# Performance work log

Measured on AMD Instinct MI355X. Metric: run time of the kernel, lower is better.

Reference implementation:

```python
import jax, jax.numpy as jnp
import numpy as np

B, D, S, F, C, H, OUT = 4, 60, 512, 158, 64, 128, 1
LN_EPS = 1e-5


def setup_inputs() -> dict:
    key = jax.random.key(0)
    ks = jax.random.split(key, 12)
    g = lambda k, shape, s=0.05: jax.random.normal(k, shape, dtype=jnp.float32) * s
    return dict(
        x=jax.random.normal(ks[0], (B, D, S, F), dtype=jnp.float32),
        feature_mask=jax.random.randint(ks[1], (B, D, S), 0, 2).astype(bool),
        wq=g(ks[2], (F, C)), bq=jnp.zeros((C,), jnp.float32),
        wk=g(ks[3], (F, C)), bk=jnp.zeros((C,), jnp.float32),
        wv=g(ks[4], (F, C)), bv=jnp.zeros((C,), jnp.float32),
        ln_g=jnp.ones((F + C,), jnp.float32), ln_b=jnp.zeros((F + C,), jnp.float32),
        w_ih=g(ks[5], (3 * H, F + C)), w_hh=g(ks[6], (3 * H, H)),
        b_ih=jnp.zeros((3 * H,), jnp.float32), b_hh=jnp.zeros((3 * H,), jnp.float32),
        w1=g(ks[7], (H, H // 2)), b1=jnp.zeros((H // 2,), jnp.float32),
        w2=g(ks[8], (H // 2, OUT)), b2=jnp.zeros((OUT,), jnp.float32),
    )


def reference(x, feature_mask, wq, bq, wk, bk, wv, bv, ln_g, ln_b,
              w_ih, w_hh, b_ih, b_hh, w1, b1, w2, b2):
    b, d, s, f = x.shape
    c = wq.shape[1]
    h_dim = w_hh.shape[1]

    # --- market context attention, vectorized over (batch, days) ---
    Q = x @ wq + bq            # (B,D,S,C)
    K = x @ wk + bk
    V = x @ wv + bv
    scores = jnp.einsum('bdsc,bdtc->bdst', Q, K) / jnp.sqrt(jnp.float32(c))
    scores = jnp.where(feature_mask[:, :, None, :], scores, -1e9)  # mask keys
    attn = jax.nn.softmax(scores, axis=-1)
    ctx = jnp.einsum('bdst,bdtc->bdsc', attn, V)       # (B,D,S,C)
    ctx = jnp.where(feature_mask[..., None], ctx, 0.0)  # mask queries
    denom = jnp.maximum(feature_mask.sum(axis=2), 1).astype(x.dtype)  # (B,D)
    market = ctx.sum(axis=2) / denom[..., None]         # (B,D,C)

    # --- concat + layernorm ---
    aug = jnp.concatenate(
        [x, jnp.broadcast_to(market[:, :, None, :], (b, d, s, c))], axis=-1)
    mu = aug.mean(-1, keepdims=True)
    var = aug.var(-1, keepdims=True)
    aug = (aug - mu) / jnp.sqrt(var + LN_EPS) * ln_g + ln_b  # (B,D,S,F+C)

    # --- GRU over days, batch = B*S independent sequences ---
    seq = aug.transpose(1, 0, 2, 3).reshape(d, b * s, f + c)  # (D, N, F+C)
    x_proj = seq @ w_ih.T + b_ih                               # (D, N, 3H)

    def step(h, xp):
        hp = h @ w_hh.T + b_hh
        xr, xz, xn = jnp.split(xp, 3, axis=-1)
        hr, hz, hn = jnp.split(hp, 3, axis=-1)
        r = jax.nn.sigmoid(xr + hr)
        z = jax.nn.sigmoid(xz + hz)
        n = jnp.tanh(xn + r * hn)
        return (1.0 - z) * n + z * h, None

    h0 = jnp.zeros((b * s, h_dim), x.dtype)
    h_last, _ = jax.lax.scan(step, h0, x_proj)  # last-step output
    h_last = h_last.reshape(b, s, h_dim)

    # --- output head (dropout inactive in eval) ---
    hid = jax.nn.relu(h_last @ w1 + b1)
    return hid @ w2 + b2  # (B, S, OUT)
```

## Files before the change

kernel.cpp:

```cpp
#include <hip/hip_runtime.h>
#include <hip/hip_bf16.h>
#include <math.h>

#define BB 4
#define DD 60
#define SS 512
#define FF 158
#define CC 64
#define HH 128
#define FC 222
#define G3 384
#define NN 2048
#define BDN 240

#define L2E  1.44269504f
#define L2E2 2.88539008f
#define QSCALE 0.18033688f

typedef _Float16 f16x8 __attribute__((ext_vector_type(8)));
typedef float f32x4 __attribute__((ext_vector_type(4)));

__device__ __forceinline__ float exp2_hw(float x){ return __builtin_amdgcn_exp2f(x); }
__device__ __forceinline__ float rcp_hw(float x){ return __builtin_amdgcn_rcpf(x); }

__global__ void prep_kernel(const float* __restrict__ w_ih,
                            const float* __restrict__ wq, const float* __restrict__ wk,
                            const float* __restrict__ wv, const float* __restrict__ w_hh,
                            _Float16* __restrict__ wf16, _Float16* __restrict__ wqkv,
                            _Float16* __restrict__ whh16){
    int idx = blockIdx.x*256 + threadIdx.x;
    if (idx < 384*224){
        int n = idx / 224, k = idx % 224;
        float sc = (n < 256) ? L2E : L2E2;
        wf16[idx] = (k < FC) ? (_Float16)(w_ih[n*FC + k] * sc) : (_Float16)0.0f;
    } else if (idx < 384*224 + 192*160){
        int i2 = idx - 384*224;
        int n = i2 / 160, k = i2 % 160;
        float v = 0.0f;
        if (k < FF){
            if (n < 64)       v = wq[k*CC + n];
            else if (n < 128) v = wk[k*CC + (n-64)];
            else              v = wv[k*CC + (n-128)];
        }
        wqkv[i2] = (_Float16)v;
    } else {
        int i3 = idx - (384*224 + 192*160);
        if (i3 < 384*128){
            int n = i3 / 128;
            float sc = (n < 256) ? L2E : L2E2;
            whh16[i3] = (_Float16)(w_hh[i3] * sc);
        }
    }
}

__global__ __launch_bounds__(256) void qkv_kernel(const float* __restrict__ x,
                           const _Float16* __restrict__ wqkv,
                           const float* __restrict__ bq, const float* __restrict__ bk,
                           const float* __restrict__ bv,
                           _Float16* __restrict__ Qh, _Float16* __restrict__ Kh,
                           float* __restrict__ V){
    __shared__ _Float16 xa[5][64][40];
    int tid  = threadIdx.x;
    int lane = tid & 63, wv = tid >> 6;
    int col  = lane & 15, quad = lane >> 4;
    int row0 = blockIdx.x * 64;

    f16x8 bfr[3][5];
    #pragma unroll
    for (int nt = 0; nt < 3; ++nt){
        int n = wv*48 + nt*16 + col;
        #pragma unroll
        for (int kq = 0; kq < 5; ++kq)
            bfr[nt][kq] = *(const f16x8*)&wqkv[n*160 + kq*32 + quad*8];
    }

    for (int i = tid; i < 64*160; i += 256){
        int r = i / 160, k = i % 160;
        float v = (k < FF) ? x[(size_t)(row0 + r)*FF + k] : 0.0f;
        xa[k >> 5][r][k & 31] = (_Float16)v;
    }
    __syncthreads();

    float bias[3];
    #pragma unroll
    for (int nt = 0; nt < 3; ++nt){
        int n = wv*48 + nt*16 + col;
        bias[nt] = (n < 64) ? bq[n] : (n < 128 ? bk[n-64] : bv[n-128]);
    }

    #pragma unroll 1
    for (int mt = 0; mt < 4; ++mt){
        f16x8 a[5];
        #pragma unroll
        for (int kq = 0; kq < 5; ++kq)
            a[kq] = *(const f16x8*)&xa[kq][mt*16 + col][quad*8];
        #pragma unroll
        for (int nt = 0; nt < 3; ++nt){
            f32x4 c = {0.0f, 0.0f, 0.0f, 0.0f};
            #pragma unroll
            for (int kq = 0; kq < 5; ++kq)
                c = __builtin_amdgcn_mfma_f32_16x16x32_f16(a[kq], bfr[nt][kq], c, 0, 0, 0);
            int n = wv*48 + nt*16 + col;
            #pragma unroll
            for (int reg = 0; reg < 4; ++reg){
                int row = row0 + mt*16 + quad*4 + reg;
                float val = c[reg] + bias[nt];
                if (n < 64)       Qh[(size_t)row*CC + n]       = (_Float16)(val * QSCALE);
                else if (n < 128) Kh[(size_t)row*CC + (n-64)]  = (_Float16)val;
                else              V [(size_t)row*CC + (n-128)] = val;
            }
        }
    }
}

__global__ __launch_bounds__(512) void attn_kernel(const _Float16* __restrict__ Qh,
                                                   const _Float16* __restrict__ Kh,
                                                   const int* __restrict__ mask,
                                                   const float* __restrict__ V,
                                                   float* __restrict__ market){
    __shared__ _Float16 kf[2][512][32];
    __shared__ float w_sh[512];
    __shared__ float mk_lds[512];

    int tid  = threadIdx.x;
    int bd   = blockIdx.x;
    int lane = tid & 63, wv = tid >> 6;
    int col  = lane & 15, quad = lane >> 4;

    const _Float16* qb = Qh + (size_t)(bd*SS)*CC;
    const _Float16* kb = Kh + (size_t)(bd*SS)*CC;

    {
        int t = tid;
        w_sh[t] = 0.0f;
        mk_lds[t] = (mask[bd*SS + t] != 0) ? 1.0f : 0.0f;
    }
    for (int i = tid; i < 4096; i += 512){
        int t = i >> 3, ch = i & 7;
        *(f16x8*)&kf[ch >> 2][t][(ch & 3)*8] = *(const f16x8*)&kb[t*CC + ch*8];
    }

    f16x8 a0[4], a1[4];
    #pragma unroll
    for (int af = 0; af < 4; ++af){
        int row = wv*64 + af*16 + col;
        a0[af] = *(const f16x8*)&qb[row*CC + quad*8];
        a1[af] = *(const f16x8*)&qb[row*CC + 32 + quad*8];
    }
    __syncthreads();

    float lacc[4][4] = {{0,0,0,0},{0,0,0,0},{0,0,0,0},{0,0,0,0}};
    #pragma unroll 2
    for (int kt = 0; kt < 32; ++kt){
        f16x8 b0 = *(const f16x8*)&kf[0][kt*16 + col][quad*8];
        f16x8 b1 = *(const f16x8*)&kf[1][kt*16 + col][quad*8];
        float mkv = mk_lds[kt*16 + col];
        #pragma unroll
        for (int af = 0; af < 4; ++af){
            f32x4 c = {0.0f, 0.0f, 0.0f, 0.0f};
            c = __builtin_amdgcn_mfma_f32_16x16x32_f16(a0[af], b0, c, 0, 0, 0);
            c = __builtin_amdgcn_mfma_f32_16x16x32_f16(a1[af], b1, c, 0, 0, 0);
            #pragma unroll
            for (int reg = 0; reg < 4; ++reg)
                lacc[af][reg] += exp2_hw(c[reg]) * mkv;
        }
    }
    float crv[4][4];
    #pragma unroll
    for (int af = 0; af < 4; ++af){
        #pragma unroll
        for (int reg = 0; reg < 4; ++reg){
            float l = lacc[af][reg];
            l += __shfl_xor(l, 1, 64);
            l += __shfl_xor(l, 2, 64);
            l += __shfl_xor(l, 4, 64);
            l += __shfl_xor(l, 8, 64);
            int row = wv*64 + af*16 + quad*4 + reg;
            crv[af][reg] = mk_lds[row] * rcp_hw(l);
        }
    }

    #pragma unroll 2
    for (int kt = 0; kt < 32; ++kt){
        f16x8 b0 = *(const f16x8*)&kf[0][kt*16 + col][quad*8];
        f16x8 b1 = *(const f16x8*)&kf[1][kt*16 + col][quad*8];
        float s = 0.0f;
        #pragma unroll
        for (int af = 0; af < 4; ++af){
            f32x4 c = {0.0f, 0.0f, 0.0f, 0.0f};
            c = __builtin_amdgcn_mfma_f32_16x16x32_f16(a0[af], b0, c, 0, 0, 0);
            c = __builtin_amdgcn_mfma_f32_16x16x32_f16(a1[af], b1, c, 0, 0, 0);
            #pragma unroll
            for (int reg = 0; reg < 4; ++reg)
                s = fmaf(exp2_hw(c[reg]), crv[af][reg], s);
        }
        s += __shfl_xor(s, 16, 64);
        s += __shfl_xor(s, 32, 64);
        if (quad == 0)
            atomicAdd(&w_sh[kt*16 + col], s);
    }
    __syncthreads();

    float* msum = (float*)kf;
    {
        int c = tid & 63, grp = tid >> 6;
        const float* vb = V + (size_t)(bd*SS)*CC;
        float acc = 0.0f;
        int t0 = grp*64;
        #pragma unroll 4
        for (int t = t0; t < t0 + 64; ++t)
            acc = fmaf(w_sh[t]*mk_lds[t], vb[(size_t)t*CC + c], acc);
        msum[grp*64 + c] = acc;
    }
    __syncthreads();
    if (tid < 64){
        float s = 0.0f;
        #pragma unroll
        for (int g = 0; g < 8; ++g) s += msum[g*64 + tid];
        float cnt = 0.0f;
        #pragma unroll
        for (int j = 0; j < 8; ++j) cnt += mk_lds[tid + 64*j];
        #pragma unroll
        for (int o = 1; o < 64; o <<= 1) cnt += __shfl_xor(cnt, o, 64);
        market[bd*CC + tid] = s * rcp_hw(fmaxf(cnt, 1.0f));
    }
}

__global__ __launch_bounds__(512, 2) void xproj_kernel(const float* __restrict__ x,
                             const float* __restrict__ market,
                             const float* __restrict__ ln_g, const float* __restrict__ ln_b,
                             const _Float16* __restrict__ wf16, const float* __restrict__ b_ih,
                             _Float16* __restrict__ XP){
    __shared__ _Float16 aug[7][64][32];
    int tid  = threadIdx.x;
    int lane = tid & 63, wv = tid >> 6;
    int col  = lane & 15, quad = lane >> 4;
    int row0 = blockIdx.x * 64;

    f16x8 bfr[3][7];
    #pragma unroll
    for (int nt = 0; nt < 3; ++nt){
        int n = wv*48 + nt*16 + col;
        #pragma unroll
        for (int kq = 0; kq < 7; ++kq)
            bfr[nt][kq] = *(const f16x8*)&wf16[n*224 + kq*32 + quad*8];
    }

    {
        int wrow = wv*8 + (lane >> 3);
        int g    = lane & 7;
        int row  = row0 + wrow;
        int d = row / NN, n = row % NN;
        int b = n >> 9, s = n & 511;
        const float* xr = &x[((size_t)((b*DD + d)*SS) + s)*FF];
        const float* mr = &market[(b*DD + d)*CC];
        float v[28];
        float sum = 0.0f, sq = 0.0f;
        #pragma unroll
        for (int j = 0; j < 28; ++j){
            int f = g + 8*j;
            float vv = 0.0f;
            if (f < FF) vv = xr[f];
            else if (f < FC) vv = mr[f - FF];
            v[j] = vv;
            sum += vv; sq += vv*vv;
        }
        sum += __shfl_xor(sum,1,64); sq += __shfl_xor(sq,1,64);
        sum += __shfl_xor(sum,2,64); sq += __shfl_xor(sq,2,64);
        sum += __shfl_xor(sum,4,64); sq += __shfl_xor(sq,4,64);
        float mu   = sum * (1.0f/222.0f);
        float var  = sq * (1.0f/222.0f) - mu*mu;
        float rstd = rsqrtf(var + 1e-5f);
        #pragma unroll
        for (int j = 0; j < 28; ++j){
            int f = g + 8*j;
            float val = (f < FC) ? ((v[j]-mu)*rstd*ln_g[f] + ln_b[f]) : 0.0f;
            aug[f>>5][wrow][f&31] = (_Float16)val;
        }
    }
    __syncthreads();

    float bias[3];
    #pragma unroll
    for (int nt = 0; nt < 3; ++nt){
        int n = wv*48 + nt*16 + col;
        bias[nt] = b_ih[n] * ((n < 256) ? L2E : L2E2);
    }
    #pragma unroll 1
    for (int mt = 0; mt < 4; ++mt){
        f16x8 a[7];
        #pragma unroll
        for (int kq = 0; kq < 7; ++kq)
            a[kq] = *(const f16x8*)&aug[kq][mt*16 + col][quad*8];
        #pragma unroll
        for (int nt = 0; nt < 3; ++nt){
            f32x4 c = {0.0f, 0.0f, 0.0f, 0.0f};
            #pragma unroll
            for (int kq = 0; kq < 7; ++kq)
                c = __builtin_amdgcn_mfma_f32_16x16x32_f16(a[kq], bfr[nt][kq], c, 0, 0, 0);
            int nn = wv*48 + nt*16 + col;
            #pragma unroll
            for (int reg = 0; reg < 4; ++reg){
                int m = quad*4 + reg;
                XP[(size_t)(row0 + mt*16 + m)*G3 + nn] = (_Float16)(c[reg] + bias[nt]);
            }
        }
    }
}

#define XLOAD(dst, base_) do{                                                   \
    _Pragma("unroll") for (int hf_ = 0; hf_ < 2; ++hf_)                         \
    _Pragma("unroll") for (int rg_ = 0; rg_ < 4; ++rg_)                         \
    _Pragma("unroll") for (int g_ = 0; g_ < 3; ++g_)                            \
        dst[hf_][rg_][g_] = (base_)[rg_*G3 + g_*HH + hf_*16];                   \
}while(0)

#define BARRIER_NODRAIN() asm volatile("s_waitcnt lgkmcnt(0)\ns_barrier" ::: "memory")

#define GRU_STEP(PRD, PWR, XC, XPF, DOPF) do{                                   \
    if (DOPF) { XLOAD(XPF, xp_d + 2*DSTR); }                                    \
    f16x8 a_[4];                                                                \
    _Pragma("unroll") for (int kq = 0; kq < 4; ++kq)                            \
        a_[kq] = *(const f16x8*)&hfrag[PRD][kq][col][quad*8];                   \
    f32x4 c_[3][2];                                                             \
    _Pragma("unroll") for (int g = 0; g < 3; ++g)                               \
    _Pragma("unroll") for (int hf = 0; hf < 2; ++hf){                           \
        f32x4 acc = {0.0f, 0.0f, 0.0f, 0.0f};                                   \
        _Pragma("unroll") for (int kq = 0; kq < 4; ++kq)                        \
            acc = __builtin_amdgcn_mfma_f32_16x16x32_f16(a_[kq], bfr[g][hf][kq], acc, 0,0,0); \
        c_[g][hf] = acc;                                                        \
    }                                                                           \
    _Pragma("unroll") for (int hf = 0; hf < 2; ++hf)                            \
    _Pragma("unroll") for (int rg = 0; rg < 4; ++rg){                           \
        float r_ = rcp_hw(1.0f + exp2_hw(-((float)XC[hf][rg][0] + c_[0][hf][rg] + bh[0][hf]))); \
        float z_ = rcp_hw(1.0f + exp2_hw(-((float)XC[hf][rg][1] + c_[1][hf][rg] + bh[1][hf]))); \
        float e_ = exp2_hw((float)XC[hf][rg][2] + r_*(c_[2][hf][rg] + bh[2][hf])); \
        float n_ = 1.0f - 2.0f*rcp_hw(e_ + 1.0f);                               \
        float h_ = n_ + z_*(hcur[hf][rg] - n_);                                 \
        hcur[hf][rg] = h_;                                                      \
        hfrag[PWR][w][quad*4 + rg][hf*16 + col] = (_Float16)h_;                 \
    }                                                                           \
    xp_d += DSTR;                                                               \
    BARRIER_NODRAIN();                                                          \
}while(0)

__global__ __launch_bounds__(256, 1) void gru_kernel(const _Float16* __restrict__ XP,
                                                     const _Float16* __restrict__ whh16,
                                                     const float* __restrict__ b_hh,
                                                     const float* __restrict__ w1, const float* __restrict__ b1,
                                                     const float* __restrict__ w2, const float* __restrict__ b2,
                                                     float* __restrict__ out){
    __shared__ _Float16 hfrag[2][4][16][40];
    __shared__ float h_sh[16][132];

    const int tid  = threadIdx.x;
    const int lane = tid & 63, w = tid >> 6;
    const int col  = lane & 15, quad = lane >> 4;
    const int row0 = blockIdx.x * 16;

    for (int i = tid; i < 2*4*16*40; i += 256)
        ((_Float16*)hfrag)[i] = (_Float16)0.0f;

    f16x8 bfr[3][2][4];
    #pragma unroll
    for (int g = 0; g < 3; ++g)
    #pragma unroll
    for (int hf = 0; hf < 2; ++hf){
        int n = g*HH + w*32 + hf*16 + col;
        #pragma unroll
        for (int kq = 0; kq < 4; ++kq)
            bfr[g][hf][kq] = *(const f16x8*)&whh16[(size_t)n*HH + kq*32 + quad*8];
    }

    float bh[3][2];
    #pragma unroll
    for (int g = 0; g < 3; ++g)
    #pragma unroll
    for (int hf = 0; hf < 2; ++hf)
        bh[g][hf] = b_hh[g*HH + w*32 + hf*16 + col] * ((g < 2) ? L2E : L2E2);

    const size_t DSTR = (size_t)NN * G3;
    const _Float16* xp_d = XP + (size_t)(row0 + quad*4)*G3 + (w*32 + col);

    _Float16 xA[2][4][3], xB[2][4][3], xC[2][4][3];
    XLOAD(xA, xp_d);
    XLOAD(xB, xp_d + DSTR);

    float hcur[2][4] = {{0,0,0,0},{0,0,0,0}};
    __syncthreads();

    #pragma unroll 1
    for (int ch = 0; ch < 10; ++ch){
        const int pf = (ch < 9);
        GRU_STEP(0, 1, xA, xC, 1);
        GRU_STEP(1, 0, xB, xA, 1);
        GRU_STEP(0, 1, xC, xB, 1);
        GRU_STEP(1, 0, xA, xC, 1);
        GRU_STEP(0, 1, xB, xA, pf);
        GRU_STEP(1, 0, xC, xB, pf);
    }

    #pragma unroll
    for (int hf = 0; hf < 2; ++hf)
    #pragma unroll
    for (int rg = 0; rg < 4; ++rg)
        h_sh[quad*4 + rg][w*32 + hf*16 + col] = hcur[hf][rg];
    __syncthreads();

    {
        int c2 = tid & 63;
        int rb = tid >> 6;
        #pragma unroll
        for (int rr = 0; rr < 4; ++rr){
            int r = rb*4 + rr;
            float acc = 0.0f;
            #pragma unroll 8
            for (int k = 0; k < 128; ++k)
                acc = fmaf(h_sh[r][k], w1[k*64 + c2], acc);
            float hid = fmaxf(acc + b1[c2], 0.0f);
            float o = hid * w2[c2];
            #pragma unroll
            for (int off = 1; off < 64; off <<= 1) o += __shfl_xor(o, off, 64);
            if (c2 == 0) out[row0 + r] = o + b2[0];
        }
    }
}

extern "C" void kernel_launch(void* const* d_in, const int* in_sizes, int n_in,
                              void* d_out, int out_size, void* d_ws, size_t ws_size,
                              hipStream_t stream) {
    const float* x    = (const float*)d_in[0];
    const int*   mask = (const int*)d_in[1];
    const float* wq   = (const float*)d_in[2];
    const float* bq   = (const float*)d_in[3];
    const float* wk   = (const float*)d_in[4];
    const float* bk   = (const float*)d_in[5];
    const float* wv   = (const float*)d_in[6];
    const float* bv   = (const float*)d_in[7];
    const float* ln_g = (const float*)d_in[8];
    const float* ln_b = (const float*)d_in[9];
    const float* w_ih = (const float*)d_in[10];
    const float* w_hh = (const float*)d_in[11];
    const float* b_ih = (const float*)d_in[12];
    const float* b_hh = (const float*)d_in[13];
    const float* w1   = (const float*)d_in[14];
    const float* b1   = (const float*)d_in[15];
    const float* w2   = (const float*)d_in[16];
    const float* b2   = (const float*)d_in[17];

    float* ws = (float*)d_ws;
    _Float16* Qh  = (_Float16*)ws;
    _Float16* Kh  = (_Float16*)(ws + 3932160);
    float*    V   = ws + 7864320;
    _Float16* XP  = (_Float16*)ws;
    float* market = ws + 23592960;
    _Float16* wf16 = (_Float16*)(ws + 23608320);
    _Float16* wqkv = (_Float16*)(ws + 23651328);
    _Float16* whh16= (_Float16*)(ws + 23666688);

    prep_kernel<<<648, 256, 0, stream>>>(w_ih, wq, wk, wv, w_hh, wf16, wqkv, whh16);
    qkv_kernel<<<1920, 256, 0, stream>>>(x, wqkv, bq, bk, bv, Qh, Kh, V);
    attn_kernel<<<240, 512, 0, stream>>>(Qh, Kh, mask, V, market);
    xproj_kernel<<<1920, 512, 0, stream>>>(x, market, ln_g, ln_b, wf16, b_ih, XP);
    gru_kernel<<<128, 256, 0, stream>>>(XP, whh16, b_hh, w1, b1, w2, b2, (float*)d_out);
}
```

Baseline: 356.8 us.

## Fold V projection into market reduction and vectorize x loads in QK kernel

Drops the materialized V tensor. The attention kernel now forms the weighted sum of the raw x rows using the attention column weights, then multiplies that pooled row by wv and adds the bias scaled by the summed weights. This uses associativity (sum w·(xWv+b) = (sum w·x)Wv + b·sum w) and removes the V GEMM, its fp32 global write and its read-back. The QK kernel also loads x with float4 reads. The cost is a serial 158-step loop over wv in 64 threads per block, plus strided reads of x inside the attention kernel.

```diff
diff --git a/kernel.cpp b/kernel.cpp
--- a/kernel.cpp
+++ b/kernel.cpp
@@ -25,26 +25,23 @@
 
 __global__ void prep_kernel(const float* __restrict__ w_ih,
                             const float* __restrict__ wq, const float* __restrict__ wk,
-                            const float* __restrict__ wv, const float* __restrict__ w_hh,
-                            _Float16* __restrict__ wf16, _Float16* __restrict__ wqkv,
+                            const float* __restrict__ w_hh,
+                            _Float16* __restrict__ wf16, _Float16* __restrict__ wqk,
                             _Float16* __restrict__ whh16){
     int idx = blockIdx.x*256 + threadIdx.x;
     if (idx < 384*224){
         int n = idx / 224, k = idx % 224;
         float sc = (n < 256) ? L2E : L2E2;
         wf16[idx] = (k < FC) ? (_Float16)(w_ih[n*FC + k] * sc) : (_Float16)0.0f;
-    } else if (idx < 384*224 + 192*160){
+    } else if (idx < 384*224 + 128*160){
         int i2 = idx - 384*224;
         int n = i2 / 160, k = i2 % 160;
         float v = 0.0f;
-        if (k < FF){
-            if (n < 64)       v = wq[k*CC + n];
-            else if (n < 128) v = wk[k*CC + (n-64)];
-            else              v = wv[k*CC + (n-128)];
-        }
-        wqkv[i2] = (_Float16)v;
+        if (k < FF)
+            v = (n < 64) ? wq[k*CC + n] : wk[k*CC + (n-64)];
+        wqk[i2] = (_Float16)v;
     } else {
-        int i3 = idx - (384*224 + 192*160);
+        int i3 = idx - (384*224 + 128*160);
         if (i3 < 384*128){
             int n = i3 / 128;
             float sc = (n < 256) ? L2E : L2E2;
@@ -53,39 +50,54 @@
     }
 }
 
-__global__ __launch_bounds__(256) void qkv_kernel(const float* __restrict__ x,
-                           const _Float16* __restrict__ wqkv,
+__global__ __launch_bounds__(256) void qk_kernel(const float* __restrict__ x,
+                           const _Float16* __restrict__ wqk,
                            const float* __restrict__ bq, const float* __restrict__ bk,
-                           const float* __restrict__ bv,
-                           _Float16* __restrict__ Qh, _Float16* __restrict__ Kh,
-                           float* __restrict__ V){
+                           _Float16* __restrict__ Qh, _Float16* __restrict__ Kh){
     __shared__ _Float16 xa[5][64][40];
     int tid  = threadIdx.x;
     int lane = tid & 63, wv = tid >> 6;
     int col  = lane & 15, quad = lane >> 4;
     int row0 = blockIdx.x * 64;
 
-    f16x8 bfr[3][5];
-    #pragma unroll
-    for (int nt = 0; nt < 3; ++nt){
-        int n = wv*48 + nt*16 + col;
+    f16x8 bfr[2][5];
+    #pragma unroll
+    for (int nt = 0; nt < 2; ++nt){
+        int n = wv*32 + nt*16 + col;
         #pragma unroll
         for (int kq = 0; kq < 5; ++kq)
-            bfr[nt][kq] = *(const f16x8*)&wqkv[n*160 + kq*32 + quad*8];
-    }
-
-    for (int i = tid; i < 64*160; i += 256){
-        int r = i / 160, k = i % 160;
-        float v = (k < FF) ? x[(size_t)(row0 + r)*FF + k] : 0.0f;
-        xa[k >> 5][r][k & 31] = (_Float16)v;
-    }
-    __syncthreads();
-
-    float bias[3];
-    #pragma unroll
-    for (int nt = 0; nt < 3; ++nt){
-        int n = wv*48 + nt*16 + col;
-        bias[nt] = (n < 64) ? bq[n] : (n < 128 ? bk[n-64] : bv[n-128]);
+            bfr[nt][kq] = *(const f16x8*)&wqk[n*160 + kq*32 + quad*8];
+    }
+
+    if (tid < 128){
+        int r = tid >> 1;
+        xa[4][r][30 + (tid & 1)] = (_Float16)0.0f;
+    }
+    {
+        const float4* xb4 = (const float4*)(x + (size_t)row0*FF);
+        #pragma unroll
+        for (int j = 0; j < 10; ++j){
+            int i = tid + j*256;
+            if (i < 2528){
+                float4 v = xb4[i];
+                int base = i*4;
+                #pragma unroll
+                for (int e = 0; e < 4; ++e){
+                    int idx = base + e;
+                    int r = idx / 158;
+                    int k = idx - r*158;
+                    xa[k >> 5][r][k & 31] = (_Float16)((&v.x)[e]);
+                }
+            }
+        }
+    }
+    __syncthreads();
+
+    float bias[2];
+    #pragma unroll
+    for (int nt = 0; nt < 2; ++nt){
+        int n = wv*32 + nt*16 + col;
+        bias[nt] = (n < 64) ? bq[n] : bk[n-64];
     }
 
     #pragma unroll 1
@@ -95,19 +107,18 @@
         for (int kq = 0; kq < 5; ++kq)
             a[kq] = *(const f16x8*)&xa[kq][mt*16 + col][quad*8];
         #pragma unroll
-        for (int nt = 0; nt < 3; ++nt){
+        for (int nt = 0; nt < 2; ++nt){
             f32x4 c = {0.0f, 0.0f, 0.0f, 0.0f};
             #pragma unroll
             for (int kq = 0; kq < 5; ++kq)
                 c = __builtin_amdgcn_mfma_f32_16x16x32_f16(a[kq], bfr[nt][kq], c, 0, 0, 0);
-            int n = wv*48 + nt*16 + col;
+            int n = wv*32 + nt*16 + col;
             #pragma unroll
             for (int reg = 0; reg < 4; ++reg){
                 int row = row0 + mt*16 + quad*4 + reg;
                 float val = c[reg] + bias[nt];
-                if (n < 64)       Qh[(size_t)row*CC + n]       = (_Float16)(val * QSCALE);
-                else if (n < 128) Kh[(size_t)row*CC + (n-64)]  = (_Float16)val;
-                else              V [(size_t)row*CC + (n-128)] = val;
+                if (n < 64) Qh[(size_t)row*CC + n]      = (_Float16)(val * QSCALE);
+                else        Kh[(size_t)row*CC + (n-64)] = (_Float16)val;
             }
         }
     }
@@ -116,7 +127,9 @@
 __global__ __launch_bounds__(512) void attn_kernel(const _Float16* __restrict__ Qh,
                                                    const _Float16* __restrict__ Kh,
                                                    const int* __restrict__ mask,
-                                                   const float* __restrict__ V,
+                                                   const float* __restrict__ x,
+                                                   const float* __restrict__ wv,
+                                                   const float* __restrict__ bv,
                                                    float* __restrict__ market){
     __shared__ _Float16 kf[2][512][32];
     __shared__ float w_sh[512];
@@ -124,7 +137,7 @@
 
     int tid  = threadIdx.x;
     int bd   = blockIdx.x;
-    int lane = tid & 63, wv = tid >> 6;
+    int lane = tid & 63, wvw = tid >> 6;
     int col  = lane & 15, quad = lane >> 4;
 
     const _Float16* qb = Qh + (size_t)(bd*SS)*CC;
@@ -143,7 +156,7 @@
     f16x8 a0[4], a1[4];
     #pragma unroll
     for (int af = 0; af < 4; ++af){
-        int row = wv*64 + af*16 + col;
+        int row = wvw*64 + af*16 + col;
         a0[af] = *(const f16x8*)&qb[row*CC + quad*8];
         a1[af] = *(const f16x8*)&qb[row*CC + 32 + quad*8];
     }
@@ -175,7 +188,7 @@
             l += __shfl_xor(l, 2, 64);
             l += __shfl_xor(l, 4, 64);
             l += __shfl_xor(l, 8, 64);
-            int row = wv*64 + af*16 + quad*4 + reg;
+            int row = wvw*64 + af*16 + quad*4 + reg;
             crv[af][reg] = mk_lds[row] * rcp_hw(l);
         }
     }
@@ -201,28 +214,42 @@
     }
     __syncthreads();
 
-    float* msum = (float*)kf;
+    w_sh[tid] *= mk_lds[tid];
+    __syncthreads();
+
+    float* part = (float*)kf;
     {
-        int c = tid & 63, grp = tid >> 6;
-        const float* vb = V + (size_t)(bd*SS)*CC;
+        int tg = tid >> 8;
+        int kk = tid & 255;
         float acc = 0.0f;
-        int t0 = grp*64;
-        #pragma unroll 4
-        for (int t = t0; t < t0 + 64; ++t)
-            acc = fmaf(w_sh[t]*mk_lds[t], vb[(size_t)t*CC + c], acc);
-        msum[grp*64 + c] = acc;
+        if (kk < FF){
+            const float* xb = x + ((size_t)bd*SS + tg*256)*FF + kk;
+            #pragma unroll 8
+            for (int t = 0; t < 256; ++t)
+                acc = fmaf(w_sh[tg*256 + t], xb[(size_t)t*FF], acc);
+        }
+        part[tg*256 + kk] = acc;
     }
     __syncthreads();
     if (tid < 64){
-        float s = 0.0f;
-        #pragma unroll
-        for (int g = 0; g < 8; ++g) s += msum[g*64 + tid];
-        float cnt = 0.0f;
-        #pragma unroll
-        for (int j = 0; j < 8; ++j) cnt += mk_lds[tid + 64*j];
-        #pragma unroll
-        for (int o = 1; o < 64; o <<= 1) cnt += __shfl_xor(cnt, o, 64);
-        market[bd*CC + tid] = s * rcp_hw(fmaxf(cnt, 1.0f));
+        int c = tid;
+        float m = 0.0f;
+        for (int k = 0; k < FF; ++k){
+            float y = part[k] + part[256 + k];
+            m = fmaf(y, wv[k*CC + c], m);
+        }
+        float cnt = 0.0f, sw = 0.0f;
+        #pragma unroll
+        for (int j = 0; j < 8; ++j){
+            cnt += mk_lds[c + 64*j];
+            sw  += w_sh[c + 64*j];
+        }
+        #pragma unroll
+        for (int o = 1; o < 64; o <<= 1){
+            cnt += __shfl_xor(cnt, o, 64);
+            sw  += __shfl_xor(sw,  o, 64);
+        }
+        market[bd*CC + c] = (m + sw*bv[c]) * rcp_hw(fmaxf(cnt, 1.0f));
     }
 }
 
@@ -451,16 +478,15 @@
     float* ws = (float*)d_ws;
     _Float16* Qh  = (_Float16*)ws;
     _Float16* Kh  = (_Float16*)(ws + 3932160);
-    float*    V   = ws + 7864320;
     _Float16* XP  = (_Float16*)ws;
     float* market = ws + 23592960;
     _Float16* wf16 = (_Float16*)(ws + 23608320);
-    _Float16* wqkv = (_Float16*)(ws + 23651328);
+    _Float16* wqk  = (_Float16*)(ws + 23651328);
     _Float16* whh16= (_Float16*)(ws + 23666688);
 
-    prep_kernel<<<648, 256, 0, stream>>>(w_ih, wq, wk, wv, w_hh, wf16, wqkv, whh16);
-    qkv_kernel<<<1920, 256, 0, stream>>>(x, wqkv, bq, bk, bv, Qh, Kh, V);
-    attn_kernel<<<240, 512, 0, stream>>>(Qh, Kh, mask, V, market);
+    prep_kernel<<<648, 256, 0, stream>>>(w_ih, wq, wk, w_hh, wf16, wqk, whh16);
+    qk_kernel<<<1920, 256, 0, stream>>>(x, wqk, bq, bk, Qh, Kh);
+    attn_kernel<<<240, 512, 0, stream>>>(Qh, Kh, mask, x, wv, bv, market);
     xproj_kernel<<<1920, 512, 0, stream>>>(x, market, ln_g, ln_b, wf16, b_ih, XP);
     gru_kernel<<<128, 256, 0, stream>>>(XP, whh16, b_hh, w1, b1, w2, b2, (float*)d_out);
 }
```

Result: faster. 346.8 us (-2.8%).
